# Performance work log

Measured on AMD Instinct MI355X. Metric: run time of the kernel, lower is better.

## Reference

```python
import jax, jax.numpy as jnp
import numpy as np
from jax import lax


def haar_dwt2(x):
    """Single-level 2D Haar (db1) DWT matching pywt sign conventions.
    x: (..., H, W) with H, W even. Returns (cA, cH, cV, cD) each (..., H/2, W/2).
    pywt db1: approx = (x0+x1)/sqrt2, detail = (x0-x1)/sqrt2; dwt2 keys:
    cH='da' (detail axis -2), cV='ad' (detail axis -1).
    """
    a = x[..., 0::2, 0::2]
    b = x[..., 0::2, 1::2]
    c = x[..., 1::2, 0::2]
    d = x[..., 1::2, 1::2]
    cA = (a + b + c + d) * 0.5
    cH = (a + b - c - d) * 0.5
    cV = (a - b + c - d) * 0.5
    cD = (a - b - c + d) * 0.5
    return cA, cH, cV, cD


def wavedec2_level2_array(x):
    """pywt.wavedec2(x, 'db1', level=2) followed by pywt.coeffs_to_array.
    x: (B, C, H, W) -> (B, C, H, W) coefficient array with layout:
      [[ [[cA2, cH2],[cV2, cD2]], cH1 ],
       [ cV1,                     cD1 ]]
    """
    cA1, cH1, cV1, cD1 = haar_dwt2(x)
    cA2, cH2, cV2, cD2 = haar_dwt2(cA1)
    lvl2 = jnp.concatenate([
        jnp.concatenate([cA2, cH2], axis=-1),
        jnp.concatenate([cV2, cD2], axis=-1),
    ], axis=-2)
    top = jnp.concatenate([lvl2, cH1], axis=-1)
    bot = jnp.concatenate([cV1, cD1], axis=-1)
    return jnp.concatenate([top, bot], axis=-2)


def setup_inputs() -> dict:
    key = jax.random.key(0)
    k1, k2, k3 = jax.random.split(key, 3)
    B, C, H = 128, 3, 224
    dim, patch = 768, 16
    x = jax.random.normal(k1, (B, C, H, H), dtype=jnp.float32)
    # Conv2d default init scale ~ 1/sqrt(fan_in)
    fan_in = C * patch * patch
    W = jax.random.normal(k2, (dim, C, patch, patch), dtype=jnp.float32) / np.sqrt(fan_in)
    b = jax.random.normal(k3, (dim,), dtype=jnp.float32) / np.sqrt(fan_in)
    return {"x": x, "W": W, "b": b}


def reference(x, W, b):
    patch = W.shape[-1]
    coeffs = wavedec2_level2_array(x)  # (B, C, H, W)
    y = lax.conv_general_dilated(
        coeffs, W,
        window_strides=(patch, patch),
        padding='VALID',
        dimension_numbers=('NCHW', 'OIHW', 'NCHW'),
    ) + b[None, :, None, None]          # (B, dim, H/p, W/p)
    B, D, Hp, Wp = y.shape
    return y.reshape(B, D, Hp * Wp).transpose(0, 2, 1)  # (B, seq, dim)
```

## Files before the change

### kernel.cpp

```cpp
#include <hip/hip_runtime.h>
#include <stdint.h>

typedef __attribute__((ext_vector_type(8))) __bf16 bf16x8;
typedef __attribute__((ext_vector_type(4))) float f32x4;

__device__ __forceinline__ unsigned short f2bf(float f) {
  union { float f; unsigned int u; } v; v.f = f;
  unsigned int u = v.u;
  return (unsigned short)((u + 0x7fffu + ((u >> 16) & 1u)) >> 16);
}

__device__ __forceinline__ void async_copy16(const void* g, void* s) {
  __builtin_amdgcn_global_load_lds(
      (__attribute__((address_space(1))) void*)const_cast<void*>(g),
      (__attribute__((address_space(3))) void*)s,
      16, 0, 0);
}

#define HAAR(a, bb, cc, dd, oA, oH, oV, oD)                                    \
  oA = 0.5f * ((a + bb) + (cc + dd));                                          \
  oH = 0.5f * ((a + bb) - (cc + dd));                                          \
  oV = 0.5f * ((a - bb) + (cc - dd));                                          \
  oD = 0.5f * ((a - bb) - (cc - dd));

__global__ __launch_bounds__(256) void convw_kernel(const float* __restrict__ W,
                                                    unsigned short* __restrict__ Wb) {
  int i = blockIdx.x * 256 + threadIdx.x;
  float4 v = ((const float4*)W)[i];
  uint2 o;
  o.x = (unsigned int)f2bf(v.x) | ((unsigned int)f2bf(v.y) << 16);
  o.y = (unsigned int)f2bf(v.z) | ((unsigned int)f2bf(v.w) << 16);
  ((uint2*)Wb)[i] = o;
}

__global__ __launch_bounds__(256) void dwt2_kernel(const float* __restrict__ x,
                                                   unsigned short* __restrict__ A) {
  int tid = blockIdx.x * 256 + threadIdx.x;
  int J = tid % 56;
  int t = tid / 56;
  int I = t % 56;
  t /= 56;
  int c = t % 3;
  int b = t / 3;

  const float* xp = x + (((size_t)t * 224 + 4 * I) * 224 + 4 * J);
  float4 r0 = *(const float4*)(xp);
  float4 r1 = *(const float4*)(xp + 224);
  float4 r2 = *(const float4*)(xp + 448);
  float4 r3 = *(const float4*)(xp + 672);

  float A1[2][2], H1[2][2], V1[2][2], D1[2][2];
  HAAR(r0.x, r0.y, r1.x, r1.y, A1[0][0], H1[0][0], V1[0][0], D1[0][0]);
  HAAR(r0.z, r0.w, r1.z, r1.w, A1[0][1], H1[0][1], V1[0][1], D1[0][1]);
  HAAR(r2.x, r2.y, r3.x, r3.y, A1[1][0], H1[1][0], V1[1][0], D1[1][0]);
  HAAR(r2.z, r2.w, r3.z, r3.w, A1[1][1], H1[1][1], V1[1][1], D1[1][1]);

  auto aidx = [&](int y, int xx) -> size_t {
    int mrow = b * 196 + (y >> 4) * 14 + (xx >> 4);
    int k = c * 256 + (y & 15) * 16 + (xx & 15);
    return (size_t)mrow * 768 + (size_t)k;
  };
  auto store2 = [&](int y, int xx, float v0, float v1) {
    unsigned int p = (unsigned int)f2bf(v0) | ((unsigned int)f2bf(v1) << 16);
    *(unsigned int*)(A + aidx(y, xx)) = p;
  };

  int y0 = 2 * I, x0 = 2 * J;
  store2(y0,           112 + x0, H1[0][0], H1[0][1]);
  store2(y0 + 1,       112 + x0, H1[1][0], H1[1][1]);
  store2(112 + y0,     x0,       V1[0][0], V1[0][1]);
  store2(112 + y0 + 1, x0,       V1[1][0], V1[1][1]);
  store2(112 + y0,     112 + x0, D1[0][0], D1[0][1]);
  store2(112 + y0 + 1, 112 + x0, D1[1][0], D1[1][1]);

  float vA2, vH2, vV2, vD2;
  HAAR(A1[0][0], A1[0][1], A1[1][0], A1[1][1], vA2, vH2, vV2, vD2);
  A[aidx(I,      J)]      = f2bf(vA2);
  A[aidx(I,      56 + J)] = f2bf(vH2);
  A[aidx(56 + I, J)]      = f2bf(vV2);
  A[aidx(56 + I, 56 + J)] = f2bf(vD2);
}

__global__ __launch_bounds__(256) void gemm_kernel(const unsigned short* __restrict__ A,
                                                   const unsigned short* __restrict__ Bt,
                                                   const float* __restrict__ bias,
                                                   float* __restrict__ C) {
  constexpr int K = 768, N = 768;
  constexpr int NT = 24;
  __shared__ unsigned short As[2][128 * 32];
  __shared__ unsigned short Bs[2][128 * 32];

  const int orig = blockIdx.x;
  const int tile = (orig & 7) * 147 + (orig >> 3);
  const int bm = tile / 6, bn = tile % 6;

  const int tid = threadIdx.x;
  const int lane = tid & 63;
  const int wave = tid >> 6;
  const int wr = wave >> 1, wc = wave & 1;
  const int mbase = bm * 128, nbase = bn * 128;

  f32x4 acc[4][4] = {};

  const int off0 = wave * 1024 + lane * 16;
  const int row0 = off0 >> 6;
  const int kc0 = (off0 >> 4) & 3;
  const unsigned short* ga0 = A + (size_t)(mbase + row0) * K + kc0 * 8;
  const unsigned short* ga1 = ga0 + (size_t)64 * K;
  const unsigned short* gb0 = Bt + (size_t)(nbase + row0) * K + kc0 * 8;
  const unsigned short* gb1 = gb0 + (size_t)64 * K;

  auto stage = [&](int buf, int kt) {
    char* sa = (char*)As + buf * 8192 + wave * 1024;
    char* sb = (char*)Bs + buf * 8192 + wave * 1024;
    const int ko = kt * 32;
    async_copy16(ga0 + ko, sa);
    async_copy16(ga1 + ko, sa + 4096);
    async_copy16(gb0 + ko, sb);
    async_copy16(gb1 + ko, sb + 4096);
  };

  const int fr = lane & 15;
  const int kq = lane >> 4;

  stage(0, 0);
  asm volatile("s_waitcnt vmcnt(0)" ::: "memory");
  __syncthreads();

  for (int kt = 0; kt < NT; ++kt) {
    const int cur = kt & 1;
    if (kt < NT - 1) stage(cur ^ 1, kt + 1);

    const unsigned short* pa = As[cur] + (wr * 64 + fr) * 32 + kq * 8;
    const unsigned short* pb = Bs[cur] + (wc * 64 + fr) * 32 + kq * 8;
    bf16x8 af[4], bv[4];
#pragma unroll
    for (int mi = 0; mi < 4; ++mi) af[mi] = *(const bf16x8*)(pa + mi * 16 * 32);
#pragma unroll
    for (int ni = 0; ni < 4; ++ni) bv[ni] = *(const bf16x8*)(pb + ni * 16 * 32);
#pragma unroll
    for (int mi = 0; mi < 4; ++mi)
#pragma unroll
      for (int ni = 0; ni < 4; ++ni)
        acc[mi][ni] = __builtin_amdgcn_mfma_f32_16x16x32_bf16(af[mi], bv[ni],
                                                              acc[mi][ni], 0, 0, 0);

    asm volatile("s_waitcnt vmcnt(0)" ::: "memory");
    __syncthreads();
  }

  const int rq = lane >> 4;
#pragma unroll
  for (int ni = 0; ni < 4; ++ni) {
    int n = nbase + wc * 64 + ni * 16 + fr;
    float bv = bias[n];
#pragma unroll
    for (int mi = 0; mi < 4; ++mi) {
      int mrow = mbase + wr * 64 + mi * 16 + rq * 4;
      f32x4 v = acc[mi][ni];
#pragma unroll
      for (int j = 0; j < 4; ++j) C[(size_t)(mrow + j) * N + n] = v[j] + bv;
    }
  }
}

extern "C" void kernel_launch(void* const* d_in, const int* in_sizes, int n_in,
                              void* d_out, int out_size, void* d_ws, size_t ws_size,
                              hipStream_t stream) {
  const float* x = (const float*)d_in[0];
  const float* W = (const float*)d_in[1];
  const float* bias = (const float*)d_in[2];
  float* out = (float*)d_out;

  unsigned short* A = (unsigned short*)d_ws;
  unsigned short* Wb = (unsigned short*)((char*)d_ws + 38535168);

  convw_kernel<<<576, 256, 0, stream>>>(W, Wb);
  dwt2_kernel<<<4704, 256, 0, stream>>>(x, A);
  gemm_kernel<<<1176, 256, 0, stream>>>(A, Wb, bias, out);
}
```

Baseline: 75.41 us.

## Replace LDS-staged GEMM with direct global register loads and 3-deep prefetch

The GEMM no longer copies tiles into shared memory with barriers. Each wave loads its MFMA fragments straight from global memory into registers, keeping four stages in flight with a prefetch distance of three k-steps, and the loop is fully unrolled with scheduling barriers. This removes LDS round trips and __syncthreads stalls. In exchange, operands that waves share are no longer reused through LDS, so global/L2 traffic doubles, each lane makes small 16-byte loads spread across rows, and register pressure rises (launch_bounds 256,2).

Result: slower. 138.5 us (+83.6%).

```diff
diff --git a/kernel.cpp b/kernel.cpp
--- a/kernel.cpp
+++ b/kernel.cpp
@@ -8,13 +8,6 @@
   union { float f; unsigned int u; } v; v.f = f;
   unsigned int u = v.u;
   return (unsigned short)((u + 0x7fffu + ((u >> 16) & 1u)) >> 16);
-}
-
-__device__ __forceinline__ void async_copy16(const void* g, void* s) {
-  __builtin_amdgcn_global_load_lds(
-      (__attribute__((address_space(1))) void*)const_cast<void*>(g),
-      (__attribute__((address_space(3))) void*)s,
-      16, 0, 0);
 }
 
 #define HAAR(a, bb, cc, dd, oA, oH, oV, oD)                                    \
@@ -81,85 +74,75 @@
   A[aidx(56 + I, 56 + J)] = f2bf(vD2);
 }
 
-__global__ __launch_bounds__(256) void gemm_kernel(const unsigned short* __restrict__ A,
-                                                   const unsigned short* __restrict__ Bt,
-                                                   const float* __restrict__ bias,
-                                                   float* __restrict__ C) {
+__global__ __launch_bounds__(256, 2) void gemm_kernel(const unsigned short* __restrict__ A,
+                                                      const unsigned short* __restrict__ Bt,
+                                                      const float* __restrict__ bias,
+                                                      float* __restrict__ C) {
   constexpr int K = 768, N = 768;
   constexpr int NT = 24;
-  __shared__ unsigned short As[2][128 * 32];
-  __shared__ unsigned short Bs[2][128 * 32];
 
   const int orig = blockIdx.x;
   const int tile = (orig & 7) * 147 + (orig >> 3);
   const int bm = tile / 6, bn = tile % 6;
 
-  const int tid = threadIdx.x;
-  const int lane = tid & 63;
-  const int wave = tid >> 6;
+  const int lane = threadIdx.x & 63;
+  const int wave = threadIdx.x >> 6;
   const int wr = wave >> 1, wc = wave & 1;
-  const int mbase = bm * 128, nbase = bn * 128;
-
-  f32x4 acc[4][4] = {};
-
-  const int off0 = wave * 1024 + lane * 16;
-  const int row0 = off0 >> 6;
-  const int kc0 = (off0 >> 4) & 3;
-  const unsigned short* ga0 = A + (size_t)(mbase + row0) * K + kc0 * 8;
-  const unsigned short* ga1 = ga0 + (size_t)64 * K;
-  const unsigned short* gb0 = Bt + (size_t)(nbase + row0) * K + kc0 * 8;
-  const unsigned short* gb1 = gb0 + (size_t)64 * K;
-
-  auto stage = [&](int buf, int kt) {
-    char* sa = (char*)As + buf * 8192 + wave * 1024;
-    char* sb = (char*)Bs + buf * 8192 + wave * 1024;
-    const int ko = kt * 32;
-    async_copy16(ga0 + ko, sa);
-    async_copy16(ga1 + ko, sa + 4096);
-    async_copy16(gb0 + ko, sb);
-    async_copy16(gb1 + ko, sb + 4096);
-  };
-
   const int fr = lane & 15;
   const int kq = lane >> 4;
 
-  stage(0, 0);
-  asm volatile("s_waitcnt vmcnt(0)" ::: "memory");
-  __syncthreads();
+  const unsigned short* pa[4];
+  const unsigned short* pb[4];
+#pragma unroll
+  for (int i = 0; i < 4; ++i) {
+    pa[i] = A + (size_t)(bm * 128 + wr * 64 + i * 16 + fr) * K + kq * 8;
+    pb[i] = Bt + (size_t)(bn * 128 + wc * 64 + i * 16 + fr) * K + kq * 8;
+  }
 
+  f32x4 acc[4][4] = {};
+  bf16x8 av[4][4], bv[4][4];
+
+#pragma unroll
+  for (int s = 0; s < 3; ++s) {
+#pragma unroll
+    for (int i = 0; i < 4; ++i) av[s][i] = *(const bf16x8*)(pa[i] + s * 32);
+#pragma unroll
+    for (int i = 0; i < 4; ++i) bv[s][i] = *(const bf16x8*)(pb[i] + s * 32);
+  }
+
+#pragma unroll
   for (int kt = 0; kt < NT; ++kt) {
-    const int cur = kt & 1;
-    if (kt < NT - 1) stage(cur ^ 1, kt + 1);
-
-    const unsigned short* pa = As[cur] + (wr * 64 + fr) * 32 + kq * 8;
-    const unsigned short* pb = Bs[cur] + (wc * 64 + fr) * 32 + kq * 8;
-    bf16x8 af[4], bv[4];
+    const int cur = kt & 3;
+    if (kt + 3 < NT) {
+      const int nx = (kt + 3) & 3;
 #pragma unroll
-    for (int mi = 0; mi < 4; ++mi) af[mi] = *(const bf16x8*)(pa + mi * 16 * 32);
+      for (int i = 0; i < 4; ++i)
+        av[nx][i] = *(const bf16x8*)(pa[i] + (kt + 3) * 32);
 #pragma unroll
-    for (int ni = 0; ni < 4; ++ni) bv[ni] = *(const bf16x8*)(pb + ni * 16 * 32);
+      for (int i = 0; i < 4; ++i)
+        bv[nx][i] = *(const bf16x8*)(pb[i] + (kt + 3) * 32);
+    }
 #pragma unroll
     for (int mi = 0; mi < 4; ++mi)
 #pragma unroll
       for (int ni = 0; ni < 4; ++ni)
-        acc[mi][ni] = __builtin_amdgcn_mfma_f32_16x16x32_bf16(af[mi], bv[ni],
-                                                              acc[mi][ni], 0, 0, 0);
-
-    asm volatile("s_waitcnt vmcnt(0)" ::: "memory");
-    __syncthreads();
+        acc[mi][ni] = __builtin_amdgcn_mfma_f32_16x16x32_bf16(
+            av[cur][mi], bv[cur][ni], acc[mi][ni], 0, 0, 0);
+    __builtin_amdgcn_sched_barrier(0);
   }
 
   const int rq = lane >> 4;
+  const int mbase = bm * 128, nbase = bn * 128;
 #pragma unroll
   for (int ni = 0; ni < 4; ++ni) {
     int n = nbase + wc * 64 + ni * 16 + fr;
-    float bv = bias[n];
+    float bb = bias[n];
 #pragma unroll
     for (int mi = 0; mi < 4; ++mi) {
       int mrow = mbase + wr * 64 + mi * 16 + rq * 4;
       f32x4 v = acc[mi][ni];
 #pragma unroll
-      for (int j = 0; j < 4; ++j) C[(size_t)(mrow + j) * N + n] = v[j] + bv;
+      for (int j = 0; j < 4; ++j) C[(size_t)(mrow + j) * N + n] = v[j] + bb;
     }
   }
 }
```
